# Kernel optimization log

Hardware: AMD Instinct MI355X
Metric: run time of the kernel (lower is better)

## Reference

```python
import jax, jax.numpy as jnp
import numpy as np
import math

B, S, D, H = 2, 2048, 1024, 16
HD = D // H  # 64


def setup_inputs() -> dict:
    key = jax.random.key(0)
    ks = jax.random.split(key, 12)
    s = 1.0 / math.sqrt(D)
    inp = {
        "x": jax.random.normal(ks[0], (B, S, D), dtype=jnp.float32),
        "Wq": jax.random.normal(ks[1], (D, D), dtype=jnp.float32) * s,
        "bq": jnp.zeros((D,), dtype=jnp.float32),
        "Wk": jax.random.normal(ks[2], (D, D), dtype=jnp.float32) * s,
        "bk": jnp.zeros((D,), dtype=jnp.float32),
        "Wv": jax.random.normal(ks[3], (D, D), dtype=jnp.float32) * s,
        "bv": jnp.zeros((D,), dtype=jnp.float32),
        "Wo": jax.random.normal(ks[4], (D, D), dtype=jnp.float32) * s,
        "bo": jnp.zeros((D,), dtype=jnp.float32),
        "cross_modal_weights": jnp.ones((3, 3), dtype=jnp.float32),
        "mask": jax.random.randint(ks[5], (B, S, S), 0, 2, dtype=jnp.int32),
        "modality_info": jax.random.randint(ks[6], (B, S), 0, 3, dtype=jnp.int64),
    }
    return inp


def reference(x, Wq, bq, Wk, bk, Wv, bv, Wo, bo, cross_modal_weights, mask, modality_info):
    b, s, d = x.shape
    # QKV projections -> [b, H, s, HD]
    q = (x @ Wq + bq).reshape(b, s, H, HD).transpose(0, 2, 1, 3)
    k = (x @ Wk + bk).reshape(b, s, H, HD).transpose(0, 2, 1, 3)
    v = (x @ Wv + bv).reshape(b, s, H, HD).transpose(0, 2, 1, 3)
    scores = jnp.einsum("bhqd,bhkd->bhqk", q, k) / math.sqrt(HD)
    # modality bias: torch uses .item() -> detached scalar
    modality_bias = jax.lax.stop_gradient(jnp.mean(cross_modal_weights))
    scores = scores + modality_bias
    # user mask [b, s, s] broadcast over heads; masked_fill(mask==0, -1e9)
    scores = jnp.where(mask[:, None, :, :] == 0, jnp.float32(-1e9), scores)
    attn = jax.nn.softmax(scores, axis=-1)
    # dropout_rate = 0.0 (eval) -> identity
    ctx = jnp.einsum("bhqk,bhkd->bhqd", attn, v)
    ctx = ctx.transpose(0, 2, 1, 3).reshape(b, s, d)
    return ctx @ Wo + bo
```

## Files before the change

kernel.cpp:

```cpp
#include <hip/hip_runtime.h>
#include <math.h>

#define Bdim 2
#define Sdim 2048
#define Ddim 1024
#define Hnum 16
#define HDdim 64
#define Kdim 1024

using short8   = __attribute__((ext_vector_type(8))) short;
using ushort8  = __attribute__((ext_vector_type(8))) unsigned short;
using ushort4v = __attribute__((ext_vector_type(4))) unsigned short;
using floatx4  = __attribute__((ext_vector_type(4))) float;
using half4    = __attribute__((ext_vector_type(4))) _Float16;
using half2v   = __attribute__((ext_vector_type(2))) _Float16;

__device__ __forceinline__ unsigned short f2bf(float f) {
    __bf16 b = (__bf16)f;
    return __builtin_bit_cast(unsigned short, b);
}

__device__ __forceinline__ void async_ld16(const unsigned short* g, unsigned short* l) {
    __builtin_amdgcn_global_load_lds(
        (const __attribute__((address_space(1))) unsigned int*)(g),
        (__attribute__((address_space(3))) unsigned int*)(l), 16, 0, 0);
}

__global__ __launch_bounds__(256) void prep_kernel(
    const float* __restrict__ x,
    const float* __restrict__ Wq, const float* __restrict__ Wk,
    const float* __restrict__ Wv, const float* __restrict__ Wo,
    const int* __restrict__ mask,
    unsigned short* __restrict__ xb, unsigned short* __restrict__ Wt,
    unsigned long long* __restrict__ packed)
{
    __shared__ float tile[64][65];
    const int bid = blockIdx.x;
    const int t   = threadIdx.x;

    if (bid < 2048) {
        size_t i = ((size_t)bid * 256 + t) * 8;
        float4 a = *(const float4*)(x + i);
        float4 b = *(const float4*)(x + i + 4);
        ushort8 o;
        o[0] = f2bf(a.x); o[1] = f2bf(a.y); o[2] = f2bf(a.z); o[3] = f2bf(a.w);
        o[4] = f2bf(b.x); o[5] = f2bf(b.y); o[6] = f2bf(b.z); o[7] = f2bf(b.w);
        *(ushort8*)(xb + i) = o;
    } else if (bid < 3072) {
        const int idx = bid - 2048;
        const int n0 = (idx & 15) * 64;
        const int k0 = ((idx >> 4) & 15) * 64;
        const int z  = idx >> 8;
        const float* W = (z == 0) ? Wq : (z == 1) ? Wk : (z == 2) ? Wv : Wo;
        unsigned short* outp = Wt + (size_t)z * Kdim * Ddim;
#pragma unroll
        for (int i = 0; i < 4; ++i) {
            int flat = i * 256 + t;
            int r = flat >> 4;
            int c = (flat & 15) * 4;
            float4 v = *(const float4*)(W + (size_t)(k0 + r) * Ddim + n0 + c);
            tile[r][c] = v.x; tile[r][c+1] = v.y; tile[r][c+2] = v.z; tile[r][c+3] = v.w;
        }
        __syncthreads();
#pragma unroll
        for (int i = 0; i < 16; ++i) {
            int flat = i * 256 + t;
            int n = flat >> 6;
            int k = flat & 63;
            outp[(size_t)(n0 + n) * Kdim + k0 + k] = f2bf(tile[k][n]);
        }
    } else {
        const int lane = t & 63;
        const int l15  = lane & 15;
        const int quad = lane >> 4;
        const unsigned int gid = (bid - 3072) * 4 + (t >> 6);
        const int b  = gid >> 14;
        const int qg = (gid >> 7) & 127;
        const int kb = gid & 127;
        int4 mv = *(const int4*)(mask + ((size_t)(b * Sdim) + qg * 16 + l15) * Sdim + kb * 16 + quad * 4);
        unsigned long long w0 = __ballot(mv.x != 0);
        unsigned long long w1 = __ballot(mv.y != 0);
        unsigned long long w2 = __ballot(mv.z != 0);
        unsigned long long w3 = __ballot(mv.w != 0);
        if (lane == 0) {
            unsigned long long* dst = packed + (size_t)gid * 4;
            dst[0] = w0; dst[1] = w1; dst[2] = w2; dst[3] = w3;
        }
    }
}

#define MFMA_NORM(MT, NT) acc[MT][NT] = __builtin_amdgcn_mfma_f32_16x16x32_bf16(af[MT], bfr[NT], acc[MT][NT], 0, 0, 0)
#define MFMA_SWAP(MT, NT) acc[MT][NT] = __builtin_amdgcn_mfma_f32_16x16x32_bf16(bfr[NT], af[MT], acc[MT][NT], 0, 0, 0)

#define GEMM_KLOOP(APTR, WPTR, NT_TILES, MFMA_STMT)                              \
    for (int kt = 0; kt < 16; ++kt) {                                            \
        const int k0 = kt * 64;                                                  \
        __syncthreads();                                                         \
        _Pragma("unroll")                                                        \
        for (int i = 0; i < 4; ++i) {                                            \
            int flat = i * 256 + t;                                              \
            int row  = flat >> 3;                                                \
            int cg   = (flat & 7) ^ (row & 7);                                   \
            async_ld16(APTR + (size_t)(m0 + row) * Kdim + k0 + cg * 8,           \
                       As + flat * 8);                                           \
        }                                                                        \
        _Pragma("unroll")                                                        \
        for (int i = 0; i < NT_TILES; ++i) {                                     \
            int flat = i * 256 + t;                                              \
            int row  = flat >> 3;                                                \
            int cg   = (flat & 7) ^ (row & 7);                                   \
            async_ld16(WPTR + (size_t)row * Kdim + k0 + cg * 8,                  \
                       Bs + flat * 8);                                           \
        }                                                                        \
        __syncthreads();                                                         \
        _Pragma("unroll")                                                        \
        for (int ks = 0; ks < 2; ++ks) {                                         \
            short8 af[4], bfr[NT_TILES];                                         \
            _Pragma("unroll")                                                    \
            for (int mt = 0; mt < 4; ++mt) {                                     \
                int row = wm * 64 + mt * 16 + l15;                               \
                int ch  = (ks * 4 + quad) ^ (row & 7);                           \
                af[mt] = *(const short8*)(As + row * 64 + ch * 8);               \
            }                                                                    \
            _Pragma("unroll")                                                    \
            for (int nt = 0; nt < NT_TILES; ++nt) {                              \
                int row = wn * (NT_TILES * 16) + nt * 16 + l15;                  \
                int ch  = (ks * 4 + quad) ^ (row & 7);                           \
                bfr[nt] = *(const short8*)(Bs + row * 64 + ch * 8);              \
            }                                                                    \
            _Pragma("unroll")                                                    \
            for (int mt = 0; mt < 4; ++mt)                                       \
                _Pragma("unroll")                                                \
                for (int nt = 0; nt < NT_TILES; ++nt)                            \
                    MFMA_STMT(mt, nt);                                           \
        }                                                                        \
    }

__global__ __launch_bounds__(256) void qkv_mfma_kernel(
    const unsigned short* __restrict__ A, const unsigned short* __restrict__ Wt,
    const float* __restrict__ bq, const float* __restrict__ bk, const float* __restrict__ bv,
    unsigned short* __restrict__ qo, unsigned short* __restrict__ ko, _Float16* __restrict__ vto)
{
    __shared__ __align__(16) unsigned short As[128 * 64];
    __shared__ __align__(16) unsigned short Bs[128 * 64];
    const int n0   = blockIdx.x * 128;
    const int m0   = blockIdx.y * 128;
    const int wsel = n0 >> 10;
    const int c0   = n0 & 1023;
    const unsigned short* Wp = Wt + (size_t)wsel * Kdim * Ddim + (size_t)c0 * Kdim;

    const int t    = threadIdx.x;
    const int lane = t & 63;
    const int w    = t >> 6;
    const int quad = lane >> 4;
    const int l15  = lane & 15;
    const int wm   = w & 1;
    const int wn   = w >> 1;
    floatx4 acc[4][4];
#pragma unroll
    for (int mt = 0; mt < 4; ++mt)
#pragma unroll
        for (int nt = 0; nt < 4; ++nt) acc[mt][nt] = (floatx4){0.f, 0.f, 0.f, 0.f};

    if (wsel < 2) {
        GEMM_KLOOP(A, Wp, 4, MFMA_SWAP)
        const float* bias = wsel ? bk : bq;
        unsigned short* outp = wsel ? ko : qo;
        const float qsc = wsel ? 1.0f : 0.18033688011112042f;
#pragma unroll
        for (int mt = 0; mt < 4; ++mt) {
            int m    = m0 + wm * 64 + mt * 16 + l15;
            int bidx = m >> 11;
            int s    = m & 2047;
#pragma unroll
            for (int nt = 0; nt < 4; ++nt) {
                int c = c0 + wn * 64 + nt * 16 + quad * 4;
                float4 bb = *(const float4*)(bias + c);
                int h  = c >> 6;
                int hd = c & 63;
                ushort4v o;
                o[0] = f2bf((acc[mt][nt][0] + bb.x) * qsc);
                o[1] = f2bf((acc[mt][nt][1] + bb.y) * qsc);
                o[2] = f2bf((acc[mt][nt][2] + bb.z) * qsc);
                o[3] = f2bf((acc[mt][nt][3] + bb.w) * qsc);
                *(ushort4v*)(outp + ((size_t)(bidx * Hnum + h) * Sdim + s) * HDdim + hd) = o;
            }
        }
    } else {
        GEMM_KLOOP(A, Wp, 4, MFMA_NORM)
#pragma unroll
        for (int nt = 0; nt < 4; ++nt) {
            int c = c0 + wn * 64 + nt * 16 + l15;
            float bb = bv[c];
            int h  = c >> 6;
            int hd = c & 63;
#pragma unroll
            for (int mt = 0; mt < 4; ++mt) {
                int m    = m0 + wm * 64 + mt * 16 + quad * 4;
                int bidx = m >> 11;
                int s    = m & 2047;
                half4 o;
#pragma unroll
                for (int r = 0; r < 4; ++r) o[r] = (_Float16)(acc[mt][nt][r] + bb);
                *(half4*)(vto + ((size_t)(bidx * Hnum + h) * HDdim + hd) * Sdim + s) = o;
            }
        }
    }
}

__global__ __launch_bounds__(256) void out_mfma_kernel(
    const unsigned short* __restrict__ A, const unsigned short* __restrict__ Wt,
    const float* __restrict__ bias, float* __restrict__ out)
{
    __shared__ __align__(16) unsigned short As[128 * 64];
    __shared__ __align__(16) unsigned short Bs[64 * 64];
    const int n0 = blockIdx.x * 64;
    const int m0 = blockIdx.y * 128;
    const unsigned short* Wp = Wt + (size_t)3 * Kdim * Ddim + (size_t)n0 * Kdim;

    const int t    = threadIdx.x;
    const int lane = t & 63;
    const int w    = t >> 6;
    const int quad = lane >> 4;
    const int l15  = lane & 15;
    const int wm   = w & 1;
    const int wn   = w >> 1;
    floatx4 acc[4][2];
#pragma unroll
    for (int mt = 0; mt < 4; ++mt)
#pragma unroll
        for (int nt = 0; nt < 2; ++nt) acc[mt][nt] = (floatx4){0.f, 0.f, 0.f, 0.f};

    GEMM_KLOOP(A, Wp, 2, MFMA_SWAP)

#pragma unroll
    for (int mt = 0; mt < 4; ++mt) {
        int m = m0 + wm * 64 + mt * 16 + l15;
#pragma unroll
        for (int nt = 0; nt < 2; ++nt) {
            int c = n0 + wn * 32 + nt * 16 + quad * 4;
            float4 bb = *(const float4*)(bias + c);
            float4 o = make_float4(acc[mt][nt][0] + bb.x, acc[mt][nt][1] + bb.y,
                                   acc[mt][nt][2] + bb.z, acc[mt][nt][3] + bb.w);
            *(float4*)(out + (size_t)m * Ddim + c) = o;
        }
    }
}

__global__ __launch_bounds__(256, 4) void attn_mfma_kernel(
    const unsigned short* __restrict__ q, const unsigned short* __restrict__ k,
    const _Float16* __restrict__ vt, const unsigned long long* __restrict__ pmask,
    unsigned short* __restrict__ ctx)
{
    __shared__ __align__(16) unsigned short Ks[2][64 * 64];
    __shared__ __align__(16) _Float16       Vs[2][64 * 64];

    const int t    = threadIdx.x;
    const int w    = t >> 6;
    const int lane = t & 63;
    const int quad = lane >> 4;
    const int l15  = lane & 15;
    const int bid  = blockIdx.x;
    const int bh   = bid & 31;
    const int qseg = bid >> 5;
    const int b    = bh >> 4;
    const int h    = bh & 15;
    const int qrow0 = qseg * 64 + w * 16;

    const unsigned short* qp = q  + (size_t)bh * Sdim * HDdim;
    const unsigned short* kp = k  + (size_t)bh * Sdim * HDdim;
    const _Float16*       vp = vt + (size_t)bh * HDdim * Sdim;

    const int qg0 = __builtin_amdgcn_readfirstlane(qrow0 >> 4);
    const unsigned long long* __restrict__ pm =
        pmask + ((size_t)(b * 128 + qg0) * 128) * 4;

    short8 qf[2];
#pragma unroll
    for (int ks = 0; ks < 2; ++ks)
        qf[ks] = *(const short8*)(qp + (size_t)(qrow0 + l15) * HDdim + ks * 32 + quad * 8);

    floatx4 acc[4];
    floatx4 accl = (floatx4){0.f, 0.f, 0.f, 0.f};
#pragma unroll
    for (int hs = 0; hs < 4; ++hs) acc[hs] = (floatx4){0.f, 0.f, 0.f, 0.f};
    const half4 ones = {(_Float16)1.f, (_Float16)1.f, (_Float16)1.f, (_Float16)1.f};

    auto stage = [&](int buf, int key0) {
#pragma unroll
        for (int i = 0; i < 2; ++i) {
            int flat = i * 256 + t;
            int row  = flat >> 3;
            int cg   = (flat & 7) ^ (row & 7);
            async_ld16(kp + (size_t)(key0 + row) * HDdim + cg * 8, &Ks[buf][flat * 8]);
        }
#pragma unroll
        for (int i = 0; i < 2; ++i) {
            int flat = i * 256 + t;
            int row  = flat >> 3;
            int cg   = (flat & 7) ^ (row & 7);
            async_ld16((const unsigned short*)(vp + (size_t)row * Sdim + key0 + cg * 8),
                       (unsigned short*)&Vs[buf][flat * 8]);
        }
    };

    stage(0, 0);

#pragma unroll 2
    for (int kt = 0; kt < 32; ++kt) {
        const int cur = kt & 1;
        __syncthreads();
        if (kt < 31) stage(cur ^ 1, (kt + 1) * 64);

        short8 kf[2][4];
#pragma unroll
        for (int ks = 0; ks < 2; ++ks)
#pragma unroll
            for (int sub = 0; sub < 4; ++sub) {
                int row = sub * 16 + l15;
                int ch  = (ks * 4 + quad) ^ (row & 7);
                kf[ks][sub] = *(const short8*)&Ks[cur][row * 64 + ch * 8];
            }
        half4 vf[4][4];
#pragma unroll
        for (int hs = 0; hs < 4; ++hs)
#pragma unroll
            for (int c = 0; c < 4; ++c) {
                int row = hs * 16 + l15;
                int cc  = c * 2 + (quad >> 1);
                int ch  = cc ^ (row & 7);
                vf[hs][c] = *(const half4*)&Vs[cur][row * 64 + ch * 8 + (quad & 1) * 4];
            }

        floatx4 sc[4];
#pragma unroll
        for (int sub = 0; sub < 4; ++sub) sc[sub] = (floatx4){0.f, 0.f, 0.f, 0.f};
#pragma unroll
        for (int ks = 0; ks < 2; ++ks)
#pragma unroll
            for (int sub = 0; sub < 4; ++sub)
                sc[sub] = __builtin_amdgcn_mfma_f32_16x16x32_bf16(
                    kf[ks][sub], qf[ks], sc[sub], 0, 0, 0);

        half4 pf[4];
        {
            const unsigned long long* __restrict__ pg = pm + kt * 16;
#pragma unroll
            for (int c = 0; c < 4; ++c) {
                float pv[4];
#pragma unroll
                for (int r = 0; r < 4; ++r) {
                    float p = exp2f(sc[c][r]);
                    unsigned long long wmask = pg[c * 4 + r];
                    asm("v_cndmask_b32 %0, 0, %1, %2" : "=v"(pv[r]) : "v"(p), "s"(wmask));
                }
                half2v lo = __builtin_bit_cast(half2v, __builtin_amdgcn_cvt_pkrtz(pv[0], pv[1]));
                half2v hi = __builtin_bit_cast(half2v, __builtin_amdgcn_cvt_pkrtz(pv[2], pv[3]));
                pf[c][0] = lo[0]; pf[c][1] = lo[1];
                pf[c][2] = hi[0]; pf[c][3] = hi[1];
            }
        }

#pragma unroll
        for (int c = 0; c < 4; ++c) {
#pragma unroll
            for (int hs = 0; hs < 4; ++hs)
                acc[hs] = __builtin_amdgcn_mfma_f32_16x16x16f16(
                    vf[hs][c], pf[c], acc[hs], 0, 0, 0);
            accl = __builtin_amdgcn_mfma_f32_16x16x16f16(
                ones, pf[c], accl, 0, 0, 0);
        }
    }

    {
        float inv = 1.0f / fmaxf(accl[0], 1e-30f);
        int row = qrow0 + l15;
#pragma unroll
        for (int hs = 0; hs < 4; ++hs) {
            ushort4v o;
#pragma unroll
            for (int r = 0; r < 4; ++r) o[r] = f2bf(acc[hs][r] * inv);
            *(ushort4v*)(ctx + (size_t)(b * Sdim + row) * Ddim + h * 64 + hs * 16 + quad * 4) = o;
        }
    }
}

extern "C" void kernel_launch(void* const* d_in, const int* in_sizes, int n_in,
                              void* d_out, int out_size, void* d_ws, size_t ws_size,
                              hipStream_t stream) {
    const float* x   = (const float*)d_in[0];
    const float* Wq  = (const float*)d_in[1];
    const float* bq  = (const float*)d_in[2];
    const float* Wk  = (const float*)d_in[3];
    const float* bk  = (const float*)d_in[4];
    const float* Wv  = (const float*)d_in[5];
    const float* bv  = (const float*)d_in[6];
    const float* Wo  = (const float*)d_in[7];
    const float* bo  = (const float*)d_in[8];
    const int*  mask = (const int*)d_in[10];
    float* out = (float*)d_out;

    char* ws = (char*)d_ws;
    unsigned short* xb  = (unsigned short*)(ws);
    unsigned short* Wt  = (unsigned short*)(ws + (size_t)8  * 1048576);
    unsigned short* qb  = (unsigned short*)(ws + (size_t)16 * 1048576);
    unsigned short* kb  = (unsigned short*)(ws + (size_t)24 * 1048576);
    _Float16*       vtb = (_Float16*)     (ws + (size_t)32 * 1048576);
    unsigned long long* pmk = (unsigned long long*)(ws + (size_t)40 * 1048576);
    unsigned short* ctxb = xb;

    prep_kernel<<<dim3(11264), 256, 0, stream>>>(x, Wq, Wk, Wv, Wo, mask, xb, Wt, pmk);
    qkv_mfma_kernel<<<dim3(24, 32), 256, 0, stream>>>(xb, Wt, bq, bk, bv, qb, kb, vtb);
    attn_mfma_kernel<<<dim3(1024), 256, 0, stream>>>(qb, kb, vtb, pmk, ctxb);
    out_mfma_kernel<<<dim3(16, 32), 256, 0, stream>>>(ctxb, Wt, bo, out);
}
```

Baseline: 244.8 us.

## Split attention keys across warps, load K directly from global, reduce partials in LDS

The attention kernel now handles 32 query rows per block instead of 64. The four warps form a 2x2 grid over query rows and key halves, and the grid doubles to 2048 blocks with a higher occupancy hint. K fragments are read straight from global memory instead of being staged in LDS, so only V remains double-buffered in shared memory. Partial accumulators and row sums from the second key-half warps are reduced through LDS at the end. This trades an extra LDS reduction and uncoalesced-ish global K reads for more parallelism and less LDS per block.

```diff
diff --git a/kernel.cpp b/kernel.cpp
--- a/kernel.cpp
+++ b/kernel.cpp
@@ -247,13 +247,13 @@
     }
 }
 
-__global__ __launch_bounds__(256, 4) void attn_mfma_kernel(
+__global__ __launch_bounds__(256, 8) void attn_mfma_kernel(
     const unsigned short* __restrict__ q, const unsigned short* __restrict__ k,
     const _Float16* __restrict__ vt, const unsigned long long* __restrict__ pmask,
     unsigned short* __restrict__ ctx)
 {
-    __shared__ __align__(16) unsigned short Ks[2][64 * 64];
-    __shared__ __align__(16) _Float16       Vs[2][64 * 64];
+    __shared__ __align__(16) _Float16 Vs[2][64 * 64];
+    __shared__ float redl[128];
 
     const int t    = threadIdx.x;
     const int w    = t >> 6;
@@ -265,15 +265,18 @@
     const int qseg = bid >> 5;
     const int b    = bh >> 4;
     const int h    = bh & 15;
-    const int qrow0 = qseg * 64 + w * 16;
+    const int wq   = w & 1;
+    const int wk   = w >> 1;
+    const int qrow0 = qseg * 32 + wq * 16;
 
     const unsigned short* qp = q  + (size_t)bh * Sdim * HDdim;
-    const unsigned short* kp = k  + (size_t)bh * Sdim * HDdim;
+    const unsigned short* kp = k  + (size_t)bh * Sdim * HDdim + (size_t)(wk * 32) * HDdim;
     const _Float16*       vp = vt + (size_t)bh * HDdim * Sdim;
 
     const int qg0 = __builtin_amdgcn_readfirstlane(qrow0 >> 4);
+    const int wku = __builtin_amdgcn_readfirstlane(wk);
     const unsigned long long* __restrict__ pm =
-        pmask + ((size_t)(b * 128 + qg0) * 128) * 4;
+        pmask + ((size_t)(b * 128 + qg0) * 128) * 4 + wku * 8;
 
     short8 qf[2];
 #pragma unroll
@@ -287,13 +290,6 @@
     const half4 ones = {(_Float16)1.f, (_Float16)1.f, (_Float16)1.f, (_Float16)1.f};
 
     auto stage = [&](int buf, int key0) {
-#pragma unroll
-        for (int i = 0; i < 2; ++i) {
-            int flat = i * 256 + t;
-            int row  = flat >> 3;
-            int cg   = (flat & 7) ^ (row & 7);
-            async_ld16(kp + (size_t)(key0 + row) * HDdim + cg * 8, &Ks[buf][flat * 8]);
-        }
 #pragma unroll
         for (int i = 0; i < 2; ++i) {
             int flat = i * 256 + t;
@@ -310,43 +306,43 @@
     for (int kt = 0; kt < 32; ++kt) {
         const int cur = kt & 1;
         __syncthreads();
+
+        short8 kf[2][2];
+#pragma unroll
+        for (int ks = 0; ks < 2; ++ks)
+#pragma unroll
+            for (int sub = 0; sub < 2; ++sub)
+                kf[ks][sub] = *(const short8*)(kp + (size_t)(kt * 64 + sub * 16 + l15) * HDdim
+                                               + ks * 32 + quad * 8);
+
         if (kt < 31) stage(cur ^ 1, (kt + 1) * 64);
 
-        short8 kf[2][4];
-#pragma unroll
-        for (int ks = 0; ks < 2; ++ks)
-#pragma unroll
-            for (int sub = 0; sub < 4; ++sub) {
-                int row = sub * 16 + l15;
-                int ch  = (ks * 4 + quad) ^ (row & 7);
-                kf[ks][sub] = *(const short8*)&Ks[cur][row * 64 + ch * 8];
-            }
-        half4 vf[4][4];
+        half4 vf[4][2];
 #pragma unroll
         for (int hs = 0; hs < 4; ++hs)
 #pragma unroll
-            for (int c = 0; c < 4; ++c) {
+            for (int c = 0; c < 2; ++c) {
                 int row = hs * 16 + l15;
-                int cc  = c * 2 + (quad >> 1);
+                int cc  = (wk * 2 + c) * 2 + (quad >> 1);
                 int ch  = cc ^ (row & 7);
                 vf[hs][c] = *(const half4*)&Vs[cur][row * 64 + ch * 8 + (quad & 1) * 4];
             }
 
-        floatx4 sc[4];
-#pragma unroll
-        for (int sub = 0; sub < 4; ++sub) sc[sub] = (floatx4){0.f, 0.f, 0.f, 0.f};
+        floatx4 sc[2];
+#pragma unroll
+        for (int sub = 0; sub < 2; ++sub) sc[sub] = (floatx4){0.f, 0.f, 0.f, 0.f};
 #pragma unroll
         for (int ks = 0; ks < 2; ++ks)
 #pragma unroll
-            for (int sub = 0; sub < 4; ++sub)
+            for (int sub = 0; sub < 2; ++sub)
                 sc[sub] = __builtin_amdgcn_mfma_f32_16x16x32_bf16(
                     kf[ks][sub], qf[ks], sc[sub], 0, 0, 0);
 
-        half4 pf[4];
+        half4 pf[2];
         {
             const unsigned long long* __restrict__ pg = pm + kt * 16;
 #pragma unroll
-            for (int c = 0; c < 4; ++c) {
+            for (int c = 0; c < 2; ++c) {
                 float pv[4];
 #pragma unroll
                 for (int r = 0; r < 4; ++r) {
@@ -362,7 +358,7 @@
         }
 
 #pragma unroll
-        for (int c = 0; c < 4; ++c) {
+        for (int c = 0; c < 2; ++c) {
 #pragma unroll
             for (int hs = 0; hs < 4; ++hs)
                 acc[hs] = __builtin_amdgcn_mfma_f32_16x16x16f16(
@@ -372,14 +368,25 @@
         }
     }
 
-    {
-        float inv = 1.0f / fmaxf(accl[0], 1e-30f);
+    __syncthreads();
+    float* red = (float*)&Vs[0][0];
+    if (wk == 1) {
+#pragma unroll
+        for (int hs = 0; hs < 4; ++hs)
+            *(floatx4*)&red[((wq * 4 + hs) * 64 + lane) * 4] = acc[hs];
+        redl[wq * 64 + lane] = accl[0];
+    }
+    __syncthreads();
+    if (wk == 0) {
+        float lsum = accl[0] + redl[wq * 64 + lane];
+        float inv  = 1.0f / fmaxf(lsum, 1e-30f);
         int row = qrow0 + l15;
 #pragma unroll
         for (int hs = 0; hs < 4; ++hs) {
+            floatx4 o4 = acc[hs] + *(const floatx4*)&red[((wq * 4 + hs) * 64 + lane) * 4];
             ushort4v o;
 #pragma unroll
-            for (int r = 0; r < 4; ++r) o[r] = f2bf(acc[hs][r] * inv);
+            for (int r = 0; r < 4; ++r) o[r] = f2bf(o4[r] * inv);
             *(ushort4v*)(ctx + (size_t)(b * Sdim + row) * Ddim + h * 64 + hs * 16 + quad * 4) = o;
         }
     }
@@ -411,6 +418,6 @@
 
     prep_kernel<<<dim3(11264), 256, 0, stream>>>(x, Wq, Wk, Wv, Wo, mask, xb, Wt, pmk);
     qkv_mfma_kernel<<<dim3(24, 32), 256, 0, stream>>>(xb, Wt, bq, bk, bv, qb, kb, vtb);
-    attn_mfma_kernel<<<dim3(1024), 256, 0, stream>>>(qb, kb, vtb, pmk, ctxb);
+    attn_mfma_kernel<<<dim3(2048), 256, 0, stream>>>(qb, kb, vtb, pmk, ctxb);
     out_mfma_kernel<<<dim3(16, 32), 256, 0, stream>>>(ctxb, Wt, bo, out);
 }
```

Measured after the change: 315.8 us. 29.0% more time.
